# Kernel tuning notes

Hardware: AMD Instinct MI355X
Metric: run time of the kernel (lower is better)

The kernel has to match this reference:

```python
import jax, jax.numpy as jnp
import numpy as np

B, N, D, H, L, M = 2, 1024, 512, 8, 4, 256
DFF = 4 * D
LN_EPS = 1e-5


def layer_norm(x, g, b):
    mu = x.mean(-1, keepdims=True)
    var = x.var(-1, keepdims=True)
    return (x - mu) * jax.lax.rsqrt(var + LN_EPS) * g + b


def setup_inputs() -> dict:
    key = jax.random.key(0)
    ks = iter(jax.random.split(key, 32))
    s = 0.02
    inp = {
        "phi": jax.random.normal(next(ks), (B, N, D), jnp.float32),
        "coords": jax.random.normal(next(ks), (B, N, 3), jnp.float32),
        # CoordinateEncoding: Gaussian Fourier modes (init_std=0.05) + linear
        "modes": 0.05 * jax.random.normal(next(ks), (M, 3), jnp.float32),
        "We": s * jax.random.normal(next(ks), (2 * M, D), jnp.float32),
        "be": jnp.zeros((D,), jnp.float32),
        # per-block attention params, stacked over L blocks
        "wq": s * jax.random.normal(next(ks), (L, D, D), jnp.float32),
        "bq": jnp.zeros((L, D), jnp.float32),
        "wk": s * jax.random.normal(next(ks), (L, D, D), jnp.float32),
        "bk": jnp.zeros((L, D), jnp.float32),
        "wv": s * jax.random.normal(next(ks), (L, D, D), jnp.float32),
        "bv": jnp.zeros((L, D), jnp.float32),
        "wo": s * jax.random.normal(next(ks), (L, D, D), jnp.float32),
        "bo": jnp.zeros((L, D), jnp.float32),
        "temp": jnp.ones((L, H), jnp.float32),  # per-head distance temperature
        "ln1_g": jnp.ones((L, D), jnp.float32),
        "ln1_b": jnp.zeros((L, D), jnp.float32),
        "ln2_g": jnp.ones((L, D), jnp.float32),
        "ln2_b": jnp.zeros((L, D), jnp.float32),
        "w1": s * jax.random.normal(next(ks), (L, D, DFF), jnp.float32),
        "b1": jnp.zeros((L, DFF), jnp.float32),
        "w2": s * jax.random.normal(next(ks), (L, DFF, D), jnp.float32),
        "b2": jnp.zeros((L, D), jnp.float32),
        "fng": jnp.ones((D,), jnp.float32),
        "fnb": jnp.zeros((D,), jnp.float32),
    }
    return inp


def reference(phi, coords, modes, We, be, wq, bq, wk, bk, wv, bv, wo, bo, temp,
              ln1_g, ln1_b, ln2_g, ln2_b, w1, b1, w2, b2, fng, fnb):
    dh = D // H
    # coordinate encoding (random Fourier features)
    phase = jnp.einsum('bnc,mc->bnm', coords, modes)            # [B,N,M]
    feats = jnp.concatenate([jnp.cos(phase), jnp.sin(phase)], -1)  # [B,N,2M]
    x = phi + feats @ We + be
    # pairwise distances with epsilon shift, std-scaled per sample
    diff = coords[:, :, None, :] - (coords + 1e-5)[:, None, :, :]
    d = jnp.sqrt(jnp.sum(diff * diff, -1))                      # [B,N,N]
    d = d / jnp.std(d, axis=(-2, -1), keepdims=True, ddof=1)
    scale = 1.0 / np.sqrt(dh)
    for l in range(L):
        y = layer_norm(x, ln1_g[l], ln1_b[l])
        q = (y @ wq[l] + bq[l]).reshape(B, N, H, dh)
        k = (y @ wk[l] + bk[l]).reshape(B, N, H, dh)
        v = (y @ wv[l] + bv[l]).reshape(B, N, H, dh)
        scores = jnp.einsum('bihd,bjhd->bhij', q, k) * scale
        scores = scores - jax.nn.softplus(temp[l])[None, :, None, None] * d[:, None]
        a = jax.nn.softmax(scores, axis=-1)                     # [B,H,N,N]
        o = jnp.einsum('bhij,bjhd->bihd', a, v).reshape(B, N, D)
        x = x + o @ wo[l] + bo[l]
        z = layer_norm(x, ln2_g[l], ln2_b[l])
        h = jax.nn.gelu(z @ w1[l] + b1[l], approximate=False)
        x = x + h @ w2[l] + b2[l]
    return layer_norm(x, fng, fnb)
```

## Files before the change

kernel.cpp:

```cpp
#include <hip/hip_runtime.h>
#include <hip/hip_bf16.h>
#include <math.h>

#define BATCH 2
#define NTOK 1024
#define DMODEL 512
#define NHEAD 8
#define DH 64
#define NLAYER 4
#define MMODES 256
#define DFFN 2048

typedef unsigned short u16;
typedef __attribute__((ext_vector_type(4))) float f4;
typedef __attribute__((ext_vector_type(8))) short b8;

__device__ __forceinline__ float bf2f(u16 u) { return __uint_as_float(((unsigned)u) << 16); }
__device__ __forceinline__ u16 f2b(float x) {
    unsigned u = __float_as_uint(x);
    return (u16)((u + 0x7FFF + ((u >> 16) & 1)) >> 16);
}
__device__ __forceinline__ float ldx(const void* p, size_t i, int f32) {
    return f32 ? ((const float*)p)[i] : bf2f(((const u16*)p)[i]);
}
__device__ __forceinline__ void async_ld16(const u16* g, u16* l) {
    __builtin_amdgcn_global_load_lds((const __attribute__((address_space(1))) void*)g,
                                     (__attribute__((address_space(3))) void*)l, 16, 0, 0);
}

__global__ __launch_bounds__(256) void detect_kernel(const void* __restrict__ probe,
                                                     int* __restrict__ flag) {
    const u16* u = (const u16*)probe;
    int big = 0, zer = 0;
    for (int t = threadIdx.x; t < 768; t += 256) {
        u16 w = u[2 * t];
        int e = (w >> 7) & 0xFF;
        if (e >= 137) big++;
        if (w == 0) zer++;
    }
    __shared__ int sb, sz;
    if (threadIdx.x == 0) { sb = 0; sz = 0; }
    __syncthreads();
    atomicAdd(&sb, big);
    atomicAdd(&sz, zer);
    __syncthreads();
    if (threadIdx.x == 0) flag[0] = (sb >= 64 || sz >= 700) ? 1 : 0;
}

__global__ __launch_bounds__(256) void cvt_all_kernel(const void* __restrict__ phi,
                                                      const void* __restrict__ coords,
                                                      float* __restrict__ xf,
                                                      float* __restrict__ cf,
                                                      const int* __restrict__ fl) {
    int f = fl[0];
    int i = blockIdx.x * 256 + threadIdx.x;
    if (i < BATCH * NTOK * DMODEL) xf[i] = ldx(phi, i, f);
    if (i < BATCH * NTOK * 3) cf[i] = ldx(coords, i, f);
}

#define OB_BE 0
#define OB_BQKV 512
#define OB_BO 6656
#define OB_B1 8704
#define OB_B2 16896
#define OB_TEMP 18944
#define OB_L1G 18976
#define OB_L1B 21024
#define OB_L2G 23072
#define OB_L2B 25120
#define OB_FNG 27168
#define OB_FNB 27680
#define OB_MODES 28192
#define OB_TOTAL 28960
__global__ __launch_bounds__(256) void pack_params(
    const void* be_, const void* bq_, const void* bk_, const void* bv_,
    const void* bo_, const void* b1_, const void* b2_, const void* temp_,
    const void* l1g_, const void* l1b_, const void* l2g_, const void* l2b_,
    const void* fng_, const void* fnb_, const void* modes_,
    float* __restrict__ out, const int* __restrict__ fl) {
    int f = fl[0];
    for (int idx = blockIdx.x * 256 + threadIdx.x; idx < OB_TOTAL; idx += gridDim.x * 256) {
        float v;
        int i = idx;
        if (i < 512) v = ldx(be_, i, f);
        else if ((i -= 512) < 6144) {
            int l = i / 1536, r = i - l * 1536;
            v = (r < 512) ? ldx(bq_, (size_t)l * 512 + r, f)
              : (r < 1024) ? ldx(bk_, (size_t)l * 512 + r - 512, f)
              : ldx(bv_, (size_t)l * 512 + r - 1024, f);
        }
        else if ((i -= 6144) < 2048) v = ldx(bo_, i, f);
        else if ((i -= 2048) < 8192) v = ldx(b1_, i, f);
        else if ((i -= 8192) < 2048) v = ldx(b2_, i, f);
        else if ((i -= 2048) < 32)   v = ldx(temp_, i, f);
        else if ((i -= 32) < 2048)   v = ldx(l1g_, i, f);
        else if ((i -= 2048) < 2048) v = ldx(l1b_, i, f);
        else if ((i -= 2048) < 2048) v = ldx(l2g_, i, f);
        else if ((i -= 2048) < 2048) v = ldx(l2b_, i, f);
        else if ((i -= 2048) < 512)  v = ldx(fng_, i, f);
        else if ((i -= 512) < 512)   v = ldx(fnb_, i, f);
        else { i -= 512; v = ldx(modes_, i, f); }
        out[idx] = v;
    }
}

__device__ __forceinline__ void tr_tile(const void* src, size_t sbase, u16* dst,
                                        size_t dbase, int R, int C, int dstRowOff,
                                        int c0, int r0, int f) {
    __shared__ float t[32][33];
    int tx = threadIdx.x & 31, ty8 = threadIdx.x >> 5;
#pragma unroll
    for (int rr = 0; rr < 4; rr++) {
        int r = r0 + ty8 + rr * 8;
        t[ty8 + rr * 8][tx] = ldx(src, sbase + (size_t)r * C + c0 + tx, f);
    }
    __syncthreads();
#pragma unroll
    for (int rr = 0; rr < 4; rr++) {
        int c = c0 + ty8 + rr * 8;
        dst[dbase + (size_t)(dstRowOff + c) * R + r0 + tx] = f2b(t[tx][ty8 + rr * 8]);
    }
}
__global__ __launch_bounds__(256) void tr_all(const void* wq_, const void* wk_, const void* wv_,
                                              const void* wo_, const void* We_,
                                              const void* w1_, const void* w2_,
                                              u16* wqkvT, u16* woT, u16* WeT,
                                              u16* w1T, u16* w2T,
                                              const int* __restrict__ fl) {
    int f = fl[0];
    int z = blockIdx.x;
    if (z < 3072) {
        int mat = z >> 8, t = z & 255;
        int l = mat / 3, m3 = mat - l * 3;
        const void* s = (m3 == 0) ? wq_ : (m3 == 1) ? wk_ : wv_;
        tr_tile(s, (size_t)l * 512 * 512, wqkvT, (size_t)l * 1536 * 512,
                512, 512, m3 * 512, (t & 15) * 32, (t >> 4) * 32, f);
    } else if (z < 4096) {
        int zz = z - 3072, l = zz >> 8, t = zz & 255;
        tr_tile(wo_, (size_t)l * 512 * 512, woT, (size_t)l * 512 * 512,
                512, 512, 0, (t & 15) * 32, (t >> 4) * 32, f);
    } else if (z < 4352) {
        int t = z - 4096;
        tr_tile(We_, 0, WeT, 0, 512, 512, 0, (t & 15) * 32, (t >> 4) * 32, f);
    } else if (z < 8448) {
        int zz = z - 4352, l = zz >> 10, t = zz & 1023;
        tr_tile(w1_, (size_t)l * 512 * 2048, w1T, (size_t)l * 2048 * 512,
                512, 2048, 0, (t & 63) * 32, (t >> 6) * 32, f);
    } else {
        int zz = z - 8448, l = zz >> 10, t = zz & 1023;
        tr_tile(w2_, (size_t)l * 2048 * 512, w2T, (size_t)l * 512 * 2048,
                2048, 512, 0, (t & 15) * 32, (t >> 4) * 32, f);
    }
}

__global__ __launch_bounds__(256) void feats_dstat(const float* __restrict__ cf,
                                                   const float* __restrict__ modesF,
                                                   u16* __restrict__ ff,
                                                   float* __restrict__ part,
                                                   u16* __restrict__ dist) {
    int row = blockIdx.x;
    {
        int m = threadIdx.x;
        float cx = cf[row * 3 + 0], cy = cf[row * 3 + 1], cz = cf[row * 3 + 2];
        float ph = cx * modesF[m * 3 + 0] + cy * modesF[m * 3 + 1] + cz * modesF[m * 3 + 2];
        ff[(size_t)row * 512 + m] = f2b(cosf(ph));
        ff[(size_t)row * 512 + MMODES + m] = f2b(sinf(ph));
    }
    int b = row >> 10, i = row & 1023;
    const float* cb = cf + (size_t)b * NTOK * 3;
    float xi = cb[i * 3], yi = cb[i * 3 + 1], zi = cb[i * 3 + 2];
    float ls = 0.f, ls2 = 0.f;
    for (int j = threadIdx.x; j < NTOK; j += 256) {
        float dx = xi - (cb[j * 3] + 1e-5f);
        float dy = yi - (cb[j * 3 + 1] + 1e-5f);
        float dz = zi - (cb[j * 3 + 2] + 1e-5f);
        float d = sqrtf(dx * dx + dy * dy + dz * dz);
        if (dist) dist[(((size_t)row) << 10) + j] = f2b(d);
        ls += d; ls2 += d * d;
    }
    for (int off = 32; off; off >>= 1) {
        ls += __shfl_down(ls, off);
        ls2 += __shfl_down(ls2, off);
    }
    __shared__ float rs[4], rs2[4];
    int wid = threadIdx.x >> 6;
    if ((threadIdx.x & 63) == 0) { rs[wid] = ls; rs2[wid] = ls2; }
    __syncthreads();
    if (threadIdx.x == 0) {
        part[row] = rs[0] + rs[1] + rs[2] + rs[3];
        part[2048 + row] = rs2[0] + rs2[1] + rs2[2] + rs2[3];
    }
}
__global__ __launch_bounds__(256) void dreduce_kernel(const float* __restrict__ part,
                                                      float* __restrict__ inv_std) {
    int b = blockIdx.x;
    double s = 0.0, s2 = 0.0;
    for (int t = threadIdx.x; t < NTOK; t += 256) {
        s += (double)part[b * NTOK + t];
        s2 += (double)part[2048 + b * NTOK + t];
    }
    for (int off = 32; off; off >>= 1) {
        s += __shfl_down(s, off);
        s2 += __shfl_down(s2, off);
    }
    __shared__ double ds[4], ds2[4];
    int wid = threadIdx.x >> 6;
    if ((threadIdx.x & 63) == 0) { ds[wid] = s; ds2[wid] = s2; }
    __syncthreads();
    if (threadIdx.x == 0) {
        double S = ds[0] + ds[1] + ds[2] + ds[3];
        double S2 = ds2[0] + ds2[1] + ds2[2] + ds2[3];
        double n = (double)NTOK * (double)NTOK;
        double mean = S / n;
        double var = (S2 - n * mean * mean) / (n - 1.0);
        inv_std[b] = (float)(1.0 / sqrt(var));
    }
}

__global__ __launch_bounds__(256) void ln_bf_kernel(const float* __restrict__ x,
                                                    const float* __restrict__ gp,
                                                    const float* __restrict__ bp,
                                                    u16* __restrict__ y) {
    int row = blockIdx.x, tid = threadIdx.x;
    const float* xr = x + (size_t)row * DMODEL;
    float v0 = xr[tid], v1 = xr[tid + 256];
    float s = v0 + v1, s2 = v0 * v0 + v1 * v1;
    for (int off = 32; off; off >>= 1) {
        s += __shfl_down(s, off);
        s2 += __shfl_down(s2, off);
    }
    __shared__ float ls[4], ls2[4];
    int wid = tid >> 6;
    if ((tid & 63) == 0) { ls[wid] = s; ls2[wid] = s2; }
    __syncthreads();
    s = ls[0] + ls[1] + ls[2] + ls[3];
    s2 = ls2[0] + ls2[1] + ls2[2] + ls2[3];
    float mean = s * (1.0f / DMODEL);
    float var = s2 * (1.0f / DMODEL) - mean * mean;
    float r = rsqrtf(var + 1e-5f);
    y[(size_t)row * DMODEL + tid] = f2b((v0 - mean) * r * gp[tid] + bp[tid]);
    y[(size_t)row * DMODEL + tid + 256] = f2b((v1 - mean) * r * gp[tid + 256] + bp[tid + 256]);
}
__global__ __launch_bounds__(256) void ln_out_kernel(const float* __restrict__ x,
                                                     const float* __restrict__ gp,
                                                     const float* __restrict__ bp,
                                                     void* __restrict__ out,
                                                     const int* __restrict__ fl) {
    int f = fl[0];
    int row = blockIdx.x, tid = threadIdx.x;
    const float* xr = x + (size_t)row * DMODEL;
    float v0 = xr[tid], v1 = xr[tid + 256];
    float s = v0 + v1, s2 = v0 * v0 + v1 * v1;
    for (int off = 32; off; off >>= 1) {
        s += __shfl_down(s, off);
        s2 += __shfl_down(s2, off);
    }
    __shared__ float ls[4], ls2[4];
    int wid = tid >> 6;
    if ((tid & 63) == 0) { ls[wid] = s; ls2[wid] = s2; }
    __syncthreads();
    s = ls[0] + ls[1] + ls[2] + ls[3];
    s2 = ls2[0] + ls2[1] + ls2[2] + ls2[3];
    float mean = s * (1.0f / DMODEL);
    float var = s2 * (1.0f / DMODEL) - mean * mean;
    float r = rsqrtf(var + 1e-5f);
    float o0 = (v0 - mean) * r * gp[tid] + bp[tid];
    float o1 = (v1 - mean) * r * gp[tid + 256] + bp[tid + 256];
    size_t i0 = (size_t)row * DMODEL + tid;
    if (f) { ((float*)out)[i0] = o0; ((float*)out)[i0 + 256] = o1; }
    else   { ((u16*)out)[i0] = f2b(o0); ((u16*)out)[i0 + 256] = f2b(o1); }
}

template <int FM, int FN, int ACT, int RES, int OUTBF, int QKV>
__global__ __launch_bounds__(256) void gemm_mfma(const u16* __restrict__ A,
                                                 const u16* __restrict__ BT,
                                                 const float* __restrict__ bias,
                                                 const float* __restrict__ res,
                                                 void* __restrict__ Cp,
                                                 u16* __restrict__ VTp,
                                                 int M, int N, int K) {
    constexpr int BM = 32 * FM, BN = 32 * FN;
    constexpr int PA = BM / 64, PB = BN / 64;
    __shared__ u16 As[2 * BM * 32];
    __shared__ u16 Bs[2 * BN * 32];
    const int m0 = blockIdx.y * BM, n0 = blockIdx.x * BN;
    const int tid = threadIdx.x, lane = tid & 63, wid = tid >> 6;
    const int wm = (wid >> 1) * (16 * FM), wn = (wid & 1) * (16 * FN);
    const int quad = lane >> 4, low = lane & 15;
    const int srow = tid >> 2, scol = (tid & 3) * 8;
    f4 acc[FM][FN] = {};
    for (int k0 = 0; k0 < K; k0 += 64) {
#pragma unroll
        for (int ks = 0; ks < 2; ks++) {
#pragma unroll
            for (int p = 0; p < PA; p++)
                async_ld16(A + (size_t)(m0 + p * 64 + srow) * K + k0 + ks * 32 + scol,
                           As + ks * BM * 32 + p * 2048 + wid * 512);
#pragma unroll
            for (int p = 0; p < PB; p++)
                async_ld16(BT + (size_t)(n0 + p * 64 + srow) * K + k0 + ks * 32 + scol,
                           Bs + ks * BN * 32 + p * 2048 + wid * 512);
        }
        __syncthreads();
#pragma unroll
        for (int ks = 0; ks < 2; ks++) {
            b8 af[FM], bfr[FN];
#pragma unroll
            for (int i = 0; i < FM; i++)
                af[i] = *(const b8*)(As + ks * BM * 32 + (wm + i * 16 + low) * 32 + quad * 8);
#pragma unroll
            for (int j = 0; j < FN; j++)
                bfr[j] = *(const b8*)(Bs + ks * BN * 32 + (wn + j * 16 + low) * 32 + quad * 8);
#pragma unroll
            for (int i = 0; i < FM; i++)
#pragma unroll
                for (int j = 0; j < FN; j++)
                    acc[i][j] = __builtin_amdgcn_mfma_f32_16x16x32_bf16(af[i], bfr[j], acc[i][j], 0, 0, 0);
        }
        __syncthreads();
    }
#pragma unroll
    for (int i = 0; i < FM; i++) {
#pragma unroll
        for (int j = 0; j < FN; j++) {
            int gn = n0 + wn + j * 16 + low;
            float bv = bias[gn];
            if (QKV && gn >= 1024) {
                int h = (gn - 1024) >> 6, d = (gn - 1024) & 63;
                int gmb = m0 + wm + i * 16 + quad * 4;
                int bb = gmb >> 10, jj = gmb & 1023;
                ushort4 pk;
                pk.x = f2b(acc[i][j][0] + bv);
                pk.y = f2b(acc[i][j][1] + bv);
                pk.z = f2b(acc[i][j][2] + bv);
                pk.w = f2b(acc[i][j][3] + bv);
                *(ushort4*)(VTp + ((size_t)(bb * 8 + h) * 64 + d) * 1024 + jj) = pk;
            } else {
#pragma unroll
                for (int r = 0; r < 4; r++) {
                    int gm = m0 + wm + i * 16 + quad * 4 + r;
                    float v = acc[i][j][r] + bv;
                    if (ACT) v = 0.5f * v * (1.0f + erff(v * 0.70710678f));
                    if (RES) v += res[(size_t)gm * N + gn];
                    if (OUTBF) ((u16*)Cp)[(size_t)gm * N + gn] = f2b(v);
                    else       ((float*)Cp)[(size_t)gm * N + gn] = v;
                }
            }
        }
    }
}

template <int USE_DIST>
__global__ __launch_bounds__(256) void attn_mfma(const u16* __restrict__ qkv,
                                                 const u16* __restrict__ VT,
                                                 const float* __restrict__ cf,
                                                 const float* __restrict__ inv_std,
                                                 const float* __restrict__ tempF, int l,
                                                 const u16* __restrict__ dist,
                                                 u16* __restrict__ o) {
    const int it = blockIdx.x, h = blockIdx.y, b = blockIdx.z;
    const int i0 = it * 32, tid = threadIdx.x;
    const int lane = tid & 63, wid = tid >> 6;
    const int g = wid >> 1, p = wid & 1;
    const int quad = lane >> 4, low = lane & 15;
    __shared__ u16 Ks[2][64][72];
    __shared__ u16 Vs[2][64][72];
    __shared__ u16 Ps[4][16][72];
    __shared__ float s_ci[32][3];
    __shared__ float s_cj[2][64][3];
    const size_t rbase = (size_t)b * NTOK;
    const u16* VTh = VT + ((size_t)(b * 8 + h)) * 65536;
    b8 qf0, qf1;
    {
        const u16* qp = qkv + (rbase + i0 + g * 16 + low) * 1536 + h * 64;
        qf0 = *(const b8*)(qp + quad * 8);
        qf1 = *(const b8*)(qp + 32 + quad * 8);
    }
    if (!USE_DIST && tid < 32) {
        s_ci[tid][0] = cf[(rbase + i0 + tid) * 3 + 0];
        s_ci[tid][1] = cf[(rbase + i0 + tid) * 3 + 1];
        s_ci[tid][2] = cf[(rbase + i0 + tid) * 3 + 2];
    }
    float t0 = tempF[l * 8 + h];
    float spw = (fmaxf(t0, 0.f) + log1pf(__expf(-fabsf(t0)))) * inv_std[b];
    float mold[4] = {-1e30f, -1e30f, -1e30f, -1e30f};
    float lsum[4] = {0.f, 0.f, 0.f, 0.f};
    f4 oacc[4] = {};
    __syncthreads();
    float cqx[4], cqy[4], cqz[4];
    const u16* drow[4];
#pragma unroll
    for (int r = 0; r < 4; r++) {
        int ii = g * 16 + quad * 4 + r;
        if (USE_DIST) drow[r] = dist + ((rbase + i0 + ii) << 10);
        else { cqx[r] = s_ci[ii][0]; cqy[r] = s_ci[ii][1]; cqz[r] = s_ci[ii][2]; }
    }
    for (int t = 0; t < 8; t++) {
        __syncthreads();
#pragma unroll
        for (int tt = 0; tt < 2; tt++) {
            int j0s = (t * 2 + tt) * 64;
            int j = tid >> 2, dc = (tid & 3) * 16;
            const u16* kp = qkv + (rbase + j0s + j) * 1536 + 512 + h * 64 + dc;
            *(uint4*)&Ks[tt][j][dc] = *(const uint4*)kp;
            *(uint4*)&Ks[tt][j][dc + 8] = *(const uint4*)(kp + 8);
            const u16* vp = VTh + (size_t)j * 1024 + j0s + dc;
            *(uint4*)&Vs[tt][j][dc] = *(const uint4*)vp;
            *(uint4*)&Vs[tt][j][dc + 8] = *(const uint4*)(vp + 8);
            if (!USE_DIST && tid < 64) {
                s_cj[tt][tid][0] = cf[(rbase + j0s + tid) * 3 + 0] + 1e-5f;
                s_cj[tt][tid][1] = cf[(rbase + j0s + tid) * 3 + 1] + 1e-5f;
                s_cj[tt][tid][2] = cf[(rbase + j0s + tid) * 3 + 2] + 1e-5f;
            }
        }
        __syncthreads();
        const int j0 = (t * 2 + p) * 64;
        f4 sacc[4] = {};
#pragma unroll
        for (int jb = 0; jb < 4; jb++) {
            b8 bk0 = *(const b8*)&Ks[p][jb * 16 + low][quad * 8];
            b8 bk1 = *(const b8*)&Ks[p][jb * 16 + low][32 + quad * 8];
            sacc[jb] = __builtin_amdgcn_mfma_f32_16x16x32_bf16(qf0, bk0, sacc[jb], 0, 0, 0);
            sacc[jb] = __builtin_amdgcn_mfma_f32_16x16x32_bf16(qf1, bk1, sacc[jb], 0, 0, 0);
        }
        float sv[4][4];
#pragma unroll
        for (int jb = 0; jb < 4; jb++) {
            int j = jb * 16 + low;
            if (USE_DIST) {
#pragma unroll
                for (int r = 0; r < 4; r++)
                    sv[jb][r] = sacc[jb][r] * 0.125f - spw * bf2f(drow[r][j0 + j]);
            } else {
                float cjx = s_cj[p][j][0], cjy = s_cj[p][j][1], cjz = s_cj[p][j][2];
#pragma unroll
                for (int r = 0; r < 4; r++) {
                    float dx = cqx[r] - cjx, dy = cqy[r] - cjy, dz = cqz[r] - cjz;
                    sv[jb][r] = sacc[jb][r] * 0.125f - spw * sqrtf(dx * dx + dy * dy + dz * dz);
                }
            }
        }
        float alpha[4];
#pragma unroll
        for (int r = 0; r < 4; r++) {
            float mx = fmaxf(fmaxf(sv[0][r], sv[1][r]), fmaxf(sv[2][r], sv[3][r]));
            mx = fmaxf(mx, __shfl_xor(mx, 1));
            mx = fmaxf(mx, __shfl_xor(mx, 2));
            mx = fmaxf(mx, __shfl_xor(mx, 4));
            mx = fmaxf(mx, __shfl_xor(mx, 8));
            float mn = fmaxf(mold[r], mx);
            alpha[r] = __expf(mold[r] - mn);
            mold[r] = mn;
            float ps = 0.f;
#pragma unroll
            for (int jb = 0; jb < 4; jb++) {
                float pp = __expf(sv[jb][r] - mn);
                Ps[wid][quad * 4 + r][jb * 16 + low] = f2b(pp);
                ps += pp;
            }
            ps += __shfl_xor(ps, 1);
            ps += __shfl_xor(ps, 2);
            ps += __shfl_xor(ps, 4);
            ps += __shfl_xor(ps, 8);
            lsum[r] = lsum[r] * alpha[r] + ps;
        }
#pragma unroll
        for (int db = 0; db < 4; db++)
#pragma unroll
            for (int r = 0; r < 4; r++) oacc[db][r] *= alpha[r];
        b8 ap0 = *(const b8*)&Ps[wid][low][quad * 8];
        b8 ap1 = *(const b8*)&Ps[wid][low][32 + quad * 8];
#pragma unroll
        for (int db = 0; db < 4; db++) {
            b8 bv0 = *(const b8*)&Vs[p][db * 16 + low][quad * 8];
            b8 bv1 = *(const b8*)&Vs[p][db * 16 + low][32 + quad * 8];
            oacc[db] = __builtin_amdgcn_mfma_f32_16x16x32_bf16(ap0, bv0, oacc[db], 0, 0, 0);
            oacc[db] = __builtin_amdgcn_mfma_f32_16x16x32_bf16(ap1, bv1, oacc[db], 0, 0, 0);
        }
    }
    __syncthreads();
    float* scr = (float*)&Ks[0][0][0];
    float* Og = scr + g * 1088;
    float* Ml = Og + 1024;
    if (p == 1) {
#pragma unroll
        for (int db = 0; db < 4; db++)
#pragma unroll
            for (int r = 0; r < 4; r++)
                Og[(quad * 4 + r) * 64 + db * 16 + low] = oacc[db][r];
        if (low == 0) {
#pragma unroll
            for (int r = 0; r < 4; r++) {
                Ml[quad * 4 + r] = mold[r];
                Ml[16 + quad * 4 + r] = lsum[r];
            }
        }
    }
    __syncthreads();
    if (p == 0) {
#pragma unroll
        for (int r = 0; r < 4; r++) {
            int row = quad * 4 + r;
            float m1 = Ml[row], l1 = Ml[16 + row];
            float mm = fmaxf(mold[r], m1);
            float a0 = __expf(mold[r] - mm), a1 = __expf(m1 - mm);
            float rl = 1.f / (lsum[r] * a0 + l1 * a1);
            u16* op = o + (rbase + i0 + g * 16 + row) * 512 + h * 64 + low;
#pragma unroll
            for (int db = 0; db < 4; db++) {
                float v = oacc[db][r] * a0 + Og[row * 64 + db * 16 + low] * a1;
                op[db * 16] = f2b(v * rl);
            }
        }
    }
}

extern "C" void kernel_launch(void* const* d_in, const int* in_sizes, int n_in,
                              void* d_out, int out_size, void* d_ws, size_t ws_size,
                              hipStream_t stream) {
    const void* phi    = d_in[0];
    const void* coords = d_in[1];
    const void* modes  = d_in[2];
    const void* We     = d_in[3];
    const void* be     = d_in[4];
    const void* wq     = d_in[5];
    const void* bq     = d_in[6];
    const void* wk     = d_in[7];
    const void* bk     = d_in[8];
    const void* wv     = d_in[9];
    const void* bv     = d_in[10];
    const void* wo     = d_in[11];
    const void* bo     = d_in[12];
    const void* temp   = d_in[13];
    const void* ln1g   = d_in[14];
    const void* ln1b   = d_in[15];
    const void* ln2g   = d_in[16];
    const void* ln2b   = d_in[17];
    const void* w1     = d_in[18];
    const void* b1     = d_in[19];
    const void* w2     = d_in[20];
    const void* b2     = d_in[21];
    const void* fng    = d_in[22];
    const void* fnb    = d_in[23];

    const int R = BATCH * NTOK;
    char* ws = (char*)d_ws;
    const size_t MB = 1u << 20;
    float* xf   = (float*)(ws);
    u16*  yf    = (u16*)(ws + 4 * MB);
    u16*  of    = (u16*)(ws + 6 * MB);
    u16*  pool  = (u16*)(ws + 8 * MB);
    u16*  ff    = pool;
    u16*  qkvb  = pool;
    u16*  VTb   = (u16*)(ws + 14 * MB);
    u16*  hf    = pool;
    u16*  WeT   = (u16*)(ws + 16 * MB);
    u16*  wqkvT = (u16*)(ws + 16 * MB + 512 * 1024);
    u16*  woT   = (u16*)(ws + 22 * MB + 512 * 1024);
    u16*  w1T   = (u16*)(ws + 24 * MB + 512 * 1024);
    u16*  w2T   = (u16*)(ws + 32 * MB + 512 * 1024);
    float* prm  = (float*)(ws + 40 * MB + 512 * 1024);
    float* cf   = (float*)(ws + 41 * MB);
    float* part = (float*)(ws + 41 * MB + 128 * 1024);
    float* inv_std = (float*)(ws + 41 * MB + 192 * 1024);
    int*   flag = (int*)(ws + 41 * MB + 192 * 1024 + 64);
    u16* dist = (ws_size >= (size_t)46 * MB) ? (u16*)(ws + 42 * MB) : nullptr;

    detect_kernel<<<1, 256, 0, stream>>>(wq, flag);
    cvt_all_kernel<<<(R * DMODEL + 255) / 256, 256, 0, stream>>>(phi, coords, xf, cf, flag);
    pack_params<<<32, 256, 0, stream>>>(be, bq, bk, bv, bo, b1, b2, temp,
                                        ln1g, ln1b, ln2g, ln2b, fng, fnb, modes, prm, flag);
    tr_all<<<12544, 256, 0, stream>>>(wq, wk, wv, wo, We, w1, w2,
                                      wqkvT, woT, WeT, w1T, w2T, flag);

    feats_dstat<<<R, 256, 0, stream>>>(cf, prm + OB_MODES, ff, part, dist);
    dreduce_kernel<<<BATCH, 256, 0, stream>>>(part, inv_std);
    gemm_mfma<2, 2, 0, 1, 0, 0><<<dim3(8, 32), 256, 0, stream>>>(
        ff, WeT, prm + OB_BE, xf, xf, nullptr, R, DMODEL, DMODEL);

    for (int l = 0; l < NLAYER; l++) {
        ln_bf_kernel<<<R, 256, 0, stream>>>(xf, prm + OB_L1G + l * 512, prm + OB_L1B + l * 512, yf);
        gemm_mfma<2, 2, 0, 0, 1, 1><<<dim3(24, 32), 256, 0, stream>>>(
            yf, wqkvT + (size_t)l * 1536 * 512, prm + OB_BQKV + l * 1536, nullptr, qkvb, VTb,
            R, 1536, DMODEL);
        if (dist)
            attn_mfma<1><<<dim3(32, NHEAD, BATCH), 256, 0, stream>>>(
                qkvb, VTb, cf, inv_std, prm + OB_TEMP, l, dist, of);
        else
            attn_mfma<0><<<dim3(32, NHEAD, BATCH), 256, 0, stream>>>(
                qkvb, VTb, cf, inv_std, prm + OB_TEMP, l, nullptr, of);
        gemm_mfma<2, 2, 0, 1, 0, 0><<<dim3(8, 32), 256, 0, stream>>>(
            of, woT + (size_t)l * 512 * 512, prm + OB_BO + l * 512, xf, xf, nullptr,
            R, DMODEL, DMODEL);
        ln_bf_kernel<<<R, 256, 0, stream>>>(xf, prm + OB_L2G + l * 512, prm + OB_L2B + l * 512, yf);
        gemm_mfma<4, 2, 1, 0, 1, 0><<<dim3(32, 16), 256, 0, stream>>>(
            yf, w1T + (size_t)l * 2048 * 512, prm + OB_B1 + l * 2048, nullptr, hf, nullptr,
            R, DFFN, DMODEL);
        gemm_mfma<2, 2, 0, 1, 0, 0><<<dim3(8, 32), 256, 0, stream>>>(
            hf, w2T + (size_t)l * 512 * 2048, prm + OB_B2 + l * 512, xf, xf, nullptr,
            R, DMODEL, DFFN);
    }
    ln_out_kernel<<<R, 256, 0, stream>>>(xf, prm + OB_FNG, prm + OB_FNB, d_out, flag);
}
```

Baseline: 517.7 us.

## Fuse layer norms into GEMM prologues via epilogue row statistics; merge prep kernels

Residual-producing GEMMs now accumulate per-row sum and sum-of-squares with atomics in their epilogue. The following QKV and FFN1 GEMMs apply layer norm on the fly while loading the fp32 activations, which removes the standalone LN kernels and the bf16 intermediate buffer. The final LN also reuses these statistics. The detect, convert and param-pack kernels are merged into one prep kernel that also zeroes the stats buffer. The trade-offs are that the A tile is now a synchronous fp32 load instead of an async bf16 LDS load, there is atomic contention, and variance is computed as E[x²]−mean² in fp32.

New measurement: 582.9 us. +12.6%, slower.

```diff
diff --git a/kernel.cpp b/kernel.cpp
--- a/kernel.cpp
+++ b/kernel.cpp
@@ -28,8 +28,7 @@
                                      (__attribute__((address_space(3))) void*)l, 16, 0, 0);
 }
 
-__global__ __launch_bounds__(256) void detect_kernel(const void* __restrict__ probe,
-                                                     int* __restrict__ flag) {
+__device__ __forceinline__ int detect_local(const void* probe) {
     const u16* u = (const u16*)probe;
     int big = 0, zer = 0;
     for (int t = threadIdx.x; t < 768; t += 256) {
@@ -44,18 +43,7 @@
     atomicAdd(&sb, big);
     atomicAdd(&sz, zer);
     __syncthreads();
-    if (threadIdx.x == 0) flag[0] = (sb >= 64 || sz >= 700) ? 1 : 0;
-}
-
-__global__ __launch_bounds__(256) void cvt_all_kernel(const void* __restrict__ phi,
-                                                      const void* __restrict__ coords,
-                                                      float* __restrict__ xf,
-                                                      float* __restrict__ cf,
-                                                      const int* __restrict__ fl) {
-    int f = fl[0];
-    int i = blockIdx.x * 256 + threadIdx.x;
-    if (i < BATCH * NTOK * DMODEL) xf[i] = ldx(phi, i, f);
-    if (i < BATCH * NTOK * 3) cf[i] = ldx(coords, i, f);
+    return (sb >= 64 || sz >= 700) ? 1 : 0;
 }
 
 #define OB_BE 0
@@ -72,35 +60,51 @@
 #define OB_FNB 27680
 #define OB_MODES 28192
 #define OB_TOTAL 28960
-__global__ __launch_bounds__(256) void pack_params(
+
+__global__ __launch_bounds__(256) void prep_kernel(
+    const void* phi, const void* coords,
     const void* be_, const void* bq_, const void* bk_, const void* bv_,
     const void* bo_, const void* b1_, const void* b2_, const void* temp_,
     const void* l1g_, const void* l1b_, const void* l2g_, const void* l2b_,
     const void* fng_, const void* fnb_, const void* modes_,
-    float* __restrict__ out, const int* __restrict__ fl) {
-    int f = fl[0];
-    for (int idx = blockIdx.x * 256 + threadIdx.x; idx < OB_TOTAL; idx += gridDim.x * 256) {
-        float v;
-        int i = idx;
-        if (i < 512) v = ldx(be_, i, f);
-        else if ((i -= 512) < 6144) {
-            int l = i / 1536, r = i - l * 1536;
-            v = (r < 512) ? ldx(bq_, (size_t)l * 512 + r, f)
-              : (r < 1024) ? ldx(bk_, (size_t)l * 512 + r - 512, f)
-              : ldx(bv_, (size_t)l * 512 + r - 1024, f);
-        }
-        else if ((i -= 6144) < 2048) v = ldx(bo_, i, f);
-        else if ((i -= 2048) < 8192) v = ldx(b1_, i, f);
-        else if ((i -= 8192) < 2048) v = ldx(b2_, i, f);
-        else if ((i -= 2048) < 32)   v = ldx(temp_, i, f);
-        else if ((i -= 32) < 2048)   v = ldx(l1g_, i, f);
-        else if ((i -= 2048) < 2048) v = ldx(l1b_, i, f);
-        else if ((i -= 2048) < 2048) v = ldx(l2g_, i, f);
-        else if ((i -= 2048) < 2048) v = ldx(l2b_, i, f);
-        else if ((i -= 2048) < 512)  v = ldx(fng_, i, f);
-        else if ((i -= 512) < 512)   v = ldx(fnb_, i, f);
-        else { i -= 512; v = ldx(modes_, i, f); }
-        out[idx] = v;
+    const void* probe,
+    float* __restrict__ xf, float* __restrict__ cf, float* __restrict__ prm,
+    float* __restrict__ sbuf, int* __restrict__ flag) {
+    int f = detect_local(probe);
+    int z = blockIdx.x, tid = threadIdx.x;
+    if (z == 0 && tid == 0) flag[0] = f;
+    if (z < 4096) {
+        int i = z * 256 + tid;
+        if (i < BATCH * NTOK * DMODEL) xf[i] = ldx(phi, i, f);
+        if (i < BATCH * NTOK * 3) cf[i] = ldx(coords, i, f);
+    } else if (z < 4210) {
+        int idx = (z - 4096) * 256 + tid;
+        if (idx < OB_TOTAL) {
+            float v;
+            int i = idx;
+            if (i < 512) v = ldx(be_, i, f);
+            else if ((i -= 512) < 6144) {
+                int l = i / 1536, r = i - l * 1536;
+                v = (r < 512) ? ldx(bq_, (size_t)l * 512 + r, f)
+                  : (r < 1024) ? ldx(bk_, (size_t)l * 512 + r - 512, f)
+                  : ldx(bv_, (size_t)l * 512 + r - 1024, f);
+            }
+            else if ((i -= 6144) < 2048) v = ldx(bo_, i, f);
+            else if ((i -= 2048) < 8192) v = ldx(b1_, i, f);
+            else if ((i -= 8192) < 2048) v = ldx(b2_, i, f);
+            else if ((i -= 2048) < 32)   v = ldx(temp_, i, f);
+            else if ((i -= 32) < 2048)   v = ldx(l1g_, i, f);
+            else if ((i -= 2048) < 2048) v = ldx(l1b_, i, f);
+            else if ((i -= 2048) < 2048) v = ldx(l2g_, i, f);
+            else if ((i -= 2048) < 2048) v = ldx(l2b_, i, f);
+            else if ((i -= 2048) < 512)  v = ldx(fng_, i, f);
+            else if ((i -= 512) < 512)   v = ldx(fnb_, i, f);
+            else { i -= 512; v = ldx(modes_, i, f); }
+            prm[idx] = v;
+        }
+    } else {
+        int idx = (z - 4210) * 256 + tid;
+        sbuf[idx] = 0.f;
     }
 }
 
@@ -217,31 +221,8 @@
     }
 }
 
-__global__ __launch_bounds__(256) void ln_bf_kernel(const float* __restrict__ x,
-                                                    const float* __restrict__ gp,
-                                                    const float* __restrict__ bp,
-                                                    u16* __restrict__ y) {
-    int row = blockIdx.x, tid = threadIdx.x;
-    const float* xr = x + (size_t)row * DMODEL;
-    float v0 = xr[tid], v1 = xr[tid + 256];
-    float s = v0 + v1, s2 = v0 * v0 + v1 * v1;
-    for (int off = 32; off; off >>= 1) {
-        s += __shfl_down(s, off);
-        s2 += __shfl_down(s2, off);
-    }
-    __shared__ float ls[4], ls2[4];
-    int wid = tid >> 6;
-    if ((tid & 63) == 0) { ls[wid] = s; ls2[wid] = s2; }
-    __syncthreads();
-    s = ls[0] + ls[1] + ls[2] + ls[3];
-    s2 = ls2[0] + ls2[1] + ls2[2] + ls2[3];
-    float mean = s * (1.0f / DMODEL);
-    float var = s2 * (1.0f / DMODEL) - mean * mean;
-    float r = rsqrtf(var + 1e-5f);
-    y[(size_t)row * DMODEL + tid] = f2b((v0 - mean) * r * gp[tid] + bp[tid]);
-    y[(size_t)row * DMODEL + tid + 256] = f2b((v1 - mean) * r * gp[tid + 256] + bp[tid + 256]);
-}
 __global__ __launch_bounds__(256) void ln_out_kernel(const float* __restrict__ x,
+                                                     const float* __restrict__ sIn,
                                                      const float* __restrict__ gp,
                                                      const float* __restrict__ bp,
                                                      void* __restrict__ out,
@@ -249,21 +230,10 @@
     int f = fl[0];
     int row = blockIdx.x, tid = threadIdx.x;
     const float* xr = x + (size_t)row * DMODEL;
+    float mean = sIn[row * 2] * (1.0f / DMODEL);
+    float var = sIn[row * 2 + 1] * (1.0f / DMODEL) - mean * mean;
+    float r = rsqrtf(var + 1e-5f);
     float v0 = xr[tid], v1 = xr[tid + 256];
-    float s = v0 + v1, s2 = v0 * v0 + v1 * v1;
-    for (int off = 32; off; off >>= 1) {
-        s += __shfl_down(s, off);
-        s2 += __shfl_down(s2, off);
-    }
-    __shared__ float ls[4], ls2[4];
-    int wid = tid >> 6;
-    if ((tid & 63) == 0) { ls[wid] = s; ls2[wid] = s2; }
-    __syncthreads();
-    s = ls[0] + ls[1] + ls[2] + ls[3];
-    s2 = ls2[0] + ls2[1] + ls2[2] + ls2[3];
-    float mean = s * (1.0f / DMODEL);
-    float var = s2 * (1.0f / DMODEL) - mean * mean;
-    float r = rsqrtf(var + 1e-5f);
     float o0 = (v0 - mean) * r * gp[tid] + bp[tid];
     float o1 = (v1 - mean) * r * gp[tid + 256] + bp[tid + 256];
     size_t i0 = (size_t)row * DMODEL + tid;
@@ -271,13 +241,17 @@
     else   { ((u16*)out)[i0] = f2b(o0); ((u16*)out)[i0 + 256] = f2b(o1); }
 }
 
-template <int FM, int FN, int ACT, int RES, int OUTBF, int QKV>
-__global__ __launch_bounds__(256) void gemm_mfma(const u16* __restrict__ A,
+template <int FM, int FN, int ACT, int RES, int OUTBF, int QKV, int LNA, int STATS>
+__global__ __launch_bounds__(256) void gemm_mfma(const void* __restrict__ A,
                                                  const u16* __restrict__ BT,
                                                  const float* __restrict__ bias,
                                                  const float* __restrict__ res,
                                                  void* __restrict__ Cp,
                                                  u16* __restrict__ VTp,
+                                                 const float* __restrict__ sIn,
+                                                 const float* __restrict__ gIn,
+                                                 const float* __restrict__ bIn,
+                                                 float* __restrict__ sOut,
                                                  int M, int N, int K) {
     constexpr int BM = 32 * FM, BN = 32 * FN;
     constexpr int PA = BM / 64, PB = BN / 64;
@@ -288,17 +262,52 @@
     const int wm = (wid >> 1) * (16 * FM), wn = (wid & 1) * (16 * FN);
     const int quad = lane >> 4, low = lane & 15;
     const int srow = tid >> 2, scol = (tid & 3) * 8;
+    float meanp[PA], rstdp[PA];
+    const float* Af = (const float*)A;
+    if (LNA) {
+#pragma unroll
+        for (int p = 0; p < PA; p++) {
+            int row = m0 + p * 64 + srow;
+            float sm = sIn[row * 2] * (1.0f / DMODEL);
+            float sq = sIn[row * 2 + 1] * (1.0f / DMODEL);
+            meanp[p] = sm;
+            rstdp[p] = rsqrtf(sq - sm * sm + 1e-5f);
+        }
+    }
     f4 acc[FM][FN] = {};
     for (int k0 = 0; k0 < K; k0 += 64) {
 #pragma unroll
         for (int ks = 0; ks < 2; ks++) {
-#pragma unroll
-            for (int p = 0; p < PA; p++)
-                async_ld16(A + (size_t)(m0 + p * 64 + srow) * K + k0 + ks * 32 + scol,
-                           As + ks * BM * 32 + p * 2048 + wid * 512);
+            int kk = k0 + ks * 32 + scol;
+#pragma unroll
+            for (int p = 0; p < PA; p++) {
+                if (LNA) {
+                    const float* xr = Af + (size_t)(m0 + p * 64 + srow) * K + kk;
+                    float4 x0 = *(const float4*)xr;
+                    float4 x1 = *(const float4*)(xr + 4);
+                    float4 g0 = *(const float4*)(gIn + kk);
+                    float4 g1 = *(const float4*)(gIn + kk + 4);
+                    float4 b0 = *(const float4*)(bIn + kk);
+                    float4 b1 = *(const float4*)(bIn + kk + 4);
+                    float mn = meanp[p], rs = rstdp[p];
+                    u16 tmp[8];
+                    tmp[0] = f2b((x0.x - mn) * rs * g0.x + b0.x);
+                    tmp[1] = f2b((x0.y - mn) * rs * g0.y + b0.y);
+                    tmp[2] = f2b((x0.z - mn) * rs * g0.z + b0.z);
+                    tmp[3] = f2b((x0.w - mn) * rs * g0.w + b0.w);
+                    tmp[4] = f2b((x1.x - mn) * rs * g1.x + b1.x);
+                    tmp[5] = f2b((x1.y - mn) * rs * g1.y + b1.y);
+                    tmp[6] = f2b((x1.z - mn) * rs * g1.z + b1.z);
+                    tmp[7] = f2b((x1.w - mn) * rs * g1.w + b1.w);
+                    *(uint4*)(As + ks * BM * 32 + p * 2048 + tid * 8) = *(uint4*)tmp;
+                } else {
+                    async_ld16((const u16*)A + (size_t)(m0 + p * 64 + srow) * K + kk,
+                               As + ks * BM * 32 + p * 2048 + wid * 512);
+                }
+            }
 #pragma unroll
             for (int p = 0; p < PB; p++)
-                async_ld16(BT + (size_t)(n0 + p * 64 + srow) * K + k0 + ks * 32 + scol,
+                async_ld16(BT + (size_t)(n0 + p * 64 + srow) * K + kk,
                            Bs + ks * BN * 32 + p * 2048 + wid * 512);
         }
         __syncthreads();
@@ -318,6 +327,13 @@
                     acc[i][j] = __builtin_amdgcn_mfma_f32_16x16x32_bf16(af[i], bfr[j], acc[i][j], 0, 0, 0);
         }
         __syncthreads();
+    }
+    float rsum[FM][4], rsq[FM][4];
+    if (STATS) {
+#pragma unroll
+        for (int i = 0; i < FM; i++)
+#pragma unroll
+            for (int r = 0; r < 4; r++) { rsum[i][r] = 0.f; rsq[i][r] = 0.f; }
     }
 #pragma unroll
     for (int i = 0; i < FM; i++) {
@@ -344,9 +360,27 @@
                     if (RES) v += res[(size_t)gm * N + gn];
                     if (OUTBF) ((u16*)Cp)[(size_t)gm * N + gn] = f2b(v);
                     else       ((float*)Cp)[(size_t)gm * N + gn] = v;
+                    if (STATS) { rsum[i][r] += v; rsq[i][r] += v * v; }
                 }
             }
         }
+    }
+    if (STATS) {
+#pragma unroll
+        for (int i = 0; i < FM; i++)
+#pragma unroll
+            for (int r = 0; r < 4; r++) {
+                float a = rsum[i][r], q = rsq[i][r];
+                a += __shfl_xor(a, 1); q += __shfl_xor(q, 1);
+                a += __shfl_xor(a, 2); q += __shfl_xor(q, 2);
+                a += __shfl_xor(a, 4); q += __shfl_xor(q, 4);
+                a += __shfl_xor(a, 8); q += __shfl_xor(q, 8);
+                if (low == 0) {
+                    int row = m0 + wm + i * 16 + quad * 4 + r;
+                    atomicAdd(&sOut[row * 2], a);
+                    atomicAdd(&sOut[row * 2 + 1], q);
+                }
+            }
     }
 }
 
@@ -547,7 +581,6 @@
     char* ws = (char*)d_ws;
     const size_t MB = 1u << 20;
     float* xf   = (float*)(ws);
-    u16*  yf    = (u16*)(ws + 4 * MB);
     u16*  of    = (u16*)(ws + 6 * MB);
     u16*  pool  = (u16*)(ws + 8 * MB);
     u16*  ff    = pool;
@@ -564,24 +597,27 @@
     float* part = (float*)(ws + 41 * MB + 128 * 1024);
     float* inv_std = (float*)(ws + 41 * MB + 192 * 1024);
     int*   flag = (int*)(ws + 41 * MB + 192 * 1024 + 64);
+    float* sbuf = (float*)(ws + 41 * MB + 256 * 1024);
     u16* dist = (ws_size >= (size_t)46 * MB) ? (u16*)(ws + 42 * MB) : nullptr;
 
-    detect_kernel<<<1, 256, 0, stream>>>(wq, flag);
-    cvt_all_kernel<<<(R * DMODEL + 255) / 256, 256, 0, stream>>>(phi, coords, xf, cf, flag);
-    pack_params<<<32, 256, 0, stream>>>(be, bq, bk, bv, bo, b1, b2, temp,
-                                        ln1g, ln1b, ln2g, ln2b, fng, fnb, modes, prm, flag);
+    prep_kernel<<<4354, 256, 0, stream>>>(phi, coords, be, bq, bk, bv, bo, b1, b2, temp,
+                                          ln1g, ln1b, ln2g, ln2b, fng, fnb, modes, wq,
+                                          xf, cf, prm, sbuf, flag);
     tr_all<<<12544, 256, 0, stream>>>(wq, wk, wv, wo, We, w1, w2,
                                       wqkvT, woT, WeT, w1T, w2T, flag);
-
     feats_dstat<<<R, 256, 0, stream>>>(cf, prm + OB_MODES, ff, part, dist);
     dreduce_kernel<<<BATCH, 256, 0, stream>>>(part, inv_std);
-    gemm_mfma<2, 2, 0, 1, 0, 0><<<dim3(8, 32), 256, 0, stream>>>(
-        ff, WeT, prm + OB_BE, xf, xf, nullptr, R, DMODEL, DMODEL);
+    gemm_mfma<2, 2, 0, 1, 0, 0, 0, 1><<<dim3(8, 32), 256, 0, stream>>>(
+        ff, WeT, prm + OB_BE, xf, xf, nullptr, nullptr, nullptr, nullptr, sbuf,
+        R, DMODEL, DMODEL);
 
     for (int l = 0; l < NLAYER; l++) {
-        ln_bf_kernel<<<R, 256, 0, stream>>>(xf, prm + OB_L1G + l * 512, prm + OB_L1B + l * 512, yf);
-        gemm_mfma<2, 2, 0, 0, 1, 1><<<dim3(24, 32), 256, 0, stream>>>(
-            yf, wqkvT + (size_t)l * 1536 * 512, prm + OB_BQKV + l * 1536, nullptr, qkvb, VTb,
+        float* Sin1 = sbuf + (size_t)(2 * l) * 4096;
+        float* Sow  = sbuf + (size_t)(2 * l + 1) * 4096;
+        float* Sow2 = sbuf + (size_t)(2 * l + 2) * 4096;
+        gemm_mfma<2, 2, 0, 0, 1, 1, 1, 0><<<dim3(24, 32), 256, 0, stream>>>(
+            xf, wqkvT + (size_t)l * 1536 * 512, prm + OB_BQKV + l * 1536, nullptr, qkvb, VTb,
+            Sin1, prm + OB_L1G + l * 512, prm + OB_L1B + l * 512, nullptr,
             R, 1536, DMODEL);
         if (dist)
             attn_mfma<1><<<dim3(32, NHEAD, BATCH), 256, 0, stream>>>(
@@ -589,16 +625,17 @@
         else
             attn_mfma<0><<<dim3(32, NHEAD, BATCH), 256, 0, stream>>>(
                 qkvb, VTb, cf, inv_std, prm + OB_TEMP, l, nullptr, of);
-        gemm_mfma<2, 2, 0, 1, 0, 0><<<dim3(8, 32), 256, 0, stream>>>(
+        gemm_mfma<2, 2, 0, 1, 0, 0, 0, 1><<<dim3(8, 32), 256, 0, stream>>>(
             of, woT + (size_t)l * 512 * 512, prm + OB_BO + l * 512, xf, xf, nullptr,
-            R, DMODEL, DMODEL);
-        ln_bf_kernel<<<R, 256, 0, stream>>>(xf, prm + OB_L2G + l * 512, prm + OB_L2B + l * 512, yf);
-        gemm_mfma<4, 2, 1, 0, 1, 0><<<dim3(32, 16), 256, 0, stream>>>(
-            yf, w1T + (size_t)l * 2048 * 512, prm + OB_B1 + l * 2048, nullptr, hf, nullptr,
+            nullptr, nullptr, nullptr, Sow, R, DMODEL, DMODEL);
+        gemm_mfma<4, 2, 1, 0, 1, 0, 1, 0><<<dim3(32, 16), 256, 0, stream>>>(
+            xf, w1T + (size_t)l * 2048 * 512, prm + OB_B1 + l * 2048, nullptr, hf, nullptr,
+            Sow, prm + OB_L2G + l * 512, prm + OB_L2B + l * 512, nullptr,
             R, DFFN, DMODEL);
-        gemm_mfma<2, 2, 0, 1, 0, 0><<<dim3(8, 32), 256, 0, stream>>>(
+        gemm_mfma<2, 2, 0, 1, 0, 0, 0, 1><<<dim3(8, 32), 256, 0, stream>>>(
             hf, w2T + (size_t)l * 512 * 2048, prm + OB_B2 + l * 512, xf, xf, nullptr,
-            R, DMODEL, DFFN);
-    }
-    ln_out_kernel<<<R, 256, 0, stream>>>(xf, prm + OB_FNG, prm + OB_FNB, d_out, flag);
-}
+            nullptr, nullptr, nullptr, Sow2, R, DMODEL, DFFN);
+    }
+    ln_out_kernel<<<R, 256, 0, stream>>>(xf, sbuf + (size_t)(2 * NLAYER) * 4096,
+                                         prm + OB_FNG, prm + OB_FNB, d_out, flag);
+}
```

## Split-K with atomic accumulation for residual GEMMs; merge prep kernels

Applied to the files above, without the earlier changes.

The Wo and W2 projections, which add into the fp32 residual stream, now run as split-K GEMMs (2 and 4 slices). Each slice atomically adds its partial sum into xf, and only slice zero adds the bias. This raises the block count from 256 so more compute units are busy, at the cost of atomic traffic and a nondeterministic summation order. Separately, the detect, convert and param-pack kernels are merged into one launch that recomputes the dtype flag in every block.

New measurement: 536.2 us. +3.6%, slower.

```diff
diff --git a/kernel.cpp b/kernel.cpp
--- a/kernel.cpp
+++ b/kernel.cpp
@@ -28,8 +28,7 @@
                                      (__attribute__((address_space(3))) void*)l, 16, 0, 0);
 }
 
-__global__ __launch_bounds__(256) void detect_kernel(const void* __restrict__ probe,
-                                                     int* __restrict__ flag) {
+__device__ __forceinline__ int detect_local(const void* probe) {
     const u16* u = (const u16*)probe;
     int big = 0, zer = 0;
     for (int t = threadIdx.x; t < 768; t += 256) {
@@ -44,18 +43,7 @@
     atomicAdd(&sb, big);
     atomicAdd(&sz, zer);
     __syncthreads();
-    if (threadIdx.x == 0) flag[0] = (sb >= 64 || sz >= 700) ? 1 : 0;
-}
-
-__global__ __launch_bounds__(256) void cvt_all_kernel(const void* __restrict__ phi,
-                                                      const void* __restrict__ coords,
-                                                      float* __restrict__ xf,
-                                                      float* __restrict__ cf,
-                                                      const int* __restrict__ fl) {
-    int f = fl[0];
-    int i = blockIdx.x * 256 + threadIdx.x;
-    if (i < BATCH * NTOK * DMODEL) xf[i] = ldx(phi, i, f);
-    if (i < BATCH * NTOK * 3) cf[i] = ldx(coords, i, f);
+    return (sb >= 64 || sz >= 700) ? 1 : 0;
 }
 
 #define OB_BE 0
@@ -72,35 +60,48 @@
 #define OB_FNB 27680
 #define OB_MODES 28192
 #define OB_TOTAL 28960
-__global__ __launch_bounds__(256) void pack_params(
+
+__global__ __launch_bounds__(256) void prep_kernel(
+    const void* phi, const void* coords,
     const void* be_, const void* bq_, const void* bk_, const void* bv_,
     const void* bo_, const void* b1_, const void* b2_, const void* temp_,
     const void* l1g_, const void* l1b_, const void* l2g_, const void* l2b_,
     const void* fng_, const void* fnb_, const void* modes_,
-    float* __restrict__ out, const int* __restrict__ fl) {
-    int f = fl[0];
-    for (int idx = blockIdx.x * 256 + threadIdx.x; idx < OB_TOTAL; idx += gridDim.x * 256) {
-        float v;
-        int i = idx;
-        if (i < 512) v = ldx(be_, i, f);
-        else if ((i -= 512) < 6144) {
-            int l = i / 1536, r = i - l * 1536;
-            v = (r < 512) ? ldx(bq_, (size_t)l * 512 + r, f)
-              : (r < 1024) ? ldx(bk_, (size_t)l * 512 + r - 512, f)
-              : ldx(bv_, (size_t)l * 512 + r - 1024, f);
-        }
-        else if ((i -= 6144) < 2048) v = ldx(bo_, i, f);
-        else if ((i -= 2048) < 8192) v = ldx(b1_, i, f);
-        else if ((i -= 8192) < 2048) v = ldx(b2_, i, f);
-        else if ((i -= 2048) < 32)   v = ldx(temp_, i, f);
-        else if ((i -= 32) < 2048)   v = ldx(l1g_, i, f);
-        else if ((i -= 2048) < 2048) v = ldx(l1b_, i, f);
-        else if ((i -= 2048) < 2048) v = ldx(l2g_, i, f);
-        else if ((i -= 2048) < 2048) v = ldx(l2b_, i, f);
-        else if ((i -= 2048) < 512)  v = ldx(fng_, i, f);
-        else if ((i -= 512) < 512)   v = ldx(fnb_, i, f);
-        else { i -= 512; v = ldx(modes_, i, f); }
-        out[idx] = v;
+    const void* probe,
+    float* __restrict__ xf, float* __restrict__ cf, float* __restrict__ prm,
+    int* __restrict__ flag) {
+    int f = detect_local(probe);
+    int z = blockIdx.x, tid = threadIdx.x;
+    if (z == 0 && tid == 0) flag[0] = f;
+    if (z < 4096) {
+        int i = z * 256 + tid;
+        if (i < BATCH * NTOK * DMODEL) xf[i] = ldx(phi, i, f);
+        if (i < BATCH * NTOK * 3) cf[i] = ldx(coords, i, f);
+    } else {
+        int idx = (z - 4096) * 256 + tid;
+        if (idx < OB_TOTAL) {
+            float v;
+            int i = idx;
+            if (i < 512) v = ldx(be_, i, f);
+            else if ((i -= 512) < 6144) {
+                int l = i / 1536, r = i - l * 1536;
+                v = (r < 512) ? ldx(bq_, (size_t)l * 512 + r, f)
+                  : (r < 1024) ? ldx(bk_, (size_t)l * 512 + r - 512, f)
+                  : ldx(bv_, (size_t)l * 512 + r - 1024, f);
+            }
+            else if ((i -= 6144) < 2048) v = ldx(bo_, i, f);
+            else if ((i -= 2048) < 8192) v = ldx(b1_, i, f);
+            else if ((i -= 8192) < 2048) v = ldx(b2_, i, f);
+            else if ((i -= 2048) < 32)   v = ldx(temp_, i, f);
+            else if ((i -= 32) < 2048)   v = ldx(l1g_, i, f);
+            else if ((i -= 2048) < 2048) v = ldx(l1b_, i, f);
+            else if ((i -= 2048) < 2048) v = ldx(l2g_, i, f);
+            else if ((i -= 2048) < 2048) v = ldx(l2b_, i, f);
+            else if ((i -= 2048) < 512)  v = ldx(fng_, i, f);
+            else if ((i -= 512) < 512)   v = ldx(fnb_, i, f);
+            else { i -= 512; v = ldx(modes_, i, f); }
+            prm[idx] = v;
+        }
     }
 }
 
@@ -271,7 +272,7 @@
     else   { ((u16*)out)[i0] = f2b(o0); ((u16*)out)[i0 + 256] = f2b(o1); }
 }
 
-template <int FM, int FN, int ACT, int RES, int OUTBF, int QKV>
+template <int FM, int FN, int ACT, int RES, int OUTBF, int QKV, int ATOM, int SPLITK>
 __global__ __launch_bounds__(256) void gemm_mfma(const u16* __restrict__ A,
                                                  const u16* __restrict__ BT,
                                                  const float* __restrict__ bias,
@@ -284,21 +285,24 @@
     __shared__ u16 As[2 * BM * 32];
     __shared__ u16 Bs[2 * BN * 32];
     const int m0 = blockIdx.y * BM, n0 = blockIdx.x * BN;
+    const int kslice = (SPLITK > 1) ? (K / SPLITK) : K;
+    const int kbeg = (SPLITK > 1) ? blockIdx.z * kslice : 0;
     const int tid = threadIdx.x, lane = tid & 63, wid = tid >> 6;
     const int wm = (wid >> 1) * (16 * FM), wn = (wid & 1) * (16 * FN);
     const int quad = lane >> 4, low = lane & 15;
     const int srow = tid >> 2, scol = (tid & 3) * 8;
     f4 acc[FM][FN] = {};
-    for (int k0 = 0; k0 < K; k0 += 64) {
+    for (int k0 = kbeg; k0 < kbeg + kslice; k0 += 64) {
 #pragma unroll
         for (int ks = 0; ks < 2; ks++) {
+            int kk = k0 + ks * 32 + scol;
 #pragma unroll
             for (int p = 0; p < PA; p++)
-                async_ld16(A + (size_t)(m0 + p * 64 + srow) * K + k0 + ks * 32 + scol,
+                async_ld16(A + (size_t)(m0 + p * 64 + srow) * K + kk,
                            As + ks * BM * 32 + p * 2048 + wid * 512);
 #pragma unroll
             for (int p = 0; p < PB; p++)
-                async_ld16(BT + (size_t)(n0 + p * 64 + srow) * K + k0 + ks * 32 + scol,
+                async_ld16(BT + (size_t)(n0 + p * 64 + srow) * K + kk,
                            Bs + ks * BN * 32 + p * 2048 + wid * 512);
         }
         __syncthreads();
@@ -335,6 +339,14 @@
                 pk.z = f2b(acc[i][j][2] + bv);
                 pk.w = f2b(acc[i][j][3] + bv);
                 *(ushort4*)(VTp + ((size_t)(bb * 8 + h) * 64 + d) * 1024 + jj) = pk;
+            } else if (ATOM) {
+#pragma unroll
+                for (int r = 0; r < 4; r++) {
+                    int gm = m0 + wm + i * 16 + quad * 4 + r;
+                    float v = acc[i][j][r];
+                    if (blockIdx.z == 0) v += bv;
+                    atomicAdd(&((float*)Cp)[(size_t)gm * N + gn], v);
+                }
             } else {
 #pragma unroll
                 for (int r = 0; r < 4; r++) {
@@ -566,21 +578,19 @@
     int*   flag = (int*)(ws + 41 * MB + 192 * 1024 + 64);
     u16* dist = (ws_size >= (size_t)46 * MB) ? (u16*)(ws + 42 * MB) : nullptr;
 
-    detect_kernel<<<1, 256, 0, stream>>>(wq, flag);
-    cvt_all_kernel<<<(R * DMODEL + 255) / 256, 256, 0, stream>>>(phi, coords, xf, cf, flag);
-    pack_params<<<32, 256, 0, stream>>>(be, bq, bk, bv, bo, b1, b2, temp,
-                                        ln1g, ln1b, ln2g, ln2b, fng, fnb, modes, prm, flag);
+    prep_kernel<<<4210, 256, 0, stream>>>(phi, coords, be, bq, bk, bv, bo, b1, b2, temp,
+                                          ln1g, ln1b, ln2g, ln2b, fng, fnb, modes, wq,
+                                          xf, cf, prm, flag);
     tr_all<<<12544, 256, 0, stream>>>(wq, wk, wv, wo, We, w1, w2,
                                       wqkvT, woT, WeT, w1T, w2T, flag);
-
     feats_dstat<<<R, 256, 0, stream>>>(cf, prm + OB_MODES, ff, part, dist);
     dreduce_kernel<<<BATCH, 256, 0, stream>>>(part, inv_std);
-    gemm_mfma<2, 2, 0, 1, 0, 0><<<dim3(8, 32), 256, 0, stream>>>(
+    gemm_mfma<2, 2, 0, 1, 0, 0, 0, 0><<<dim3(8, 32), 256, 0, stream>>>(
         ff, WeT, prm + OB_BE, xf, xf, nullptr, R, DMODEL, DMODEL);
 
     for (int l = 0; l < NLAYER; l++) {
         ln_bf_kernel<<<R, 256, 0, stream>>>(xf, prm + OB_L1G + l * 512, prm + OB_L1B + l * 512, yf);
-        gemm_mfma<2, 2, 0, 0, 1, 1><<<dim3(24, 32), 256, 0, stream>>>(
+        gemm_mfma<2, 2, 0, 0, 1, 1, 0, 0><<<dim3(24, 32), 256, 0, stream>>>(
             yf, wqkvT + (size_t)l * 1536 * 512, prm + OB_BQKV + l * 1536, nullptr, qkvb, VTb,
             R, 1536, DMODEL);
         if (dist)
@@ -589,15 +599,15 @@
         else
             attn_mfma<0><<<dim3(32, NHEAD, BATCH), 256, 0, stream>>>(
                 qkvb, VTb, cf, inv_std, prm + OB_TEMP, l, nullptr, of);
-        gemm_mfma<2, 2, 0, 1, 0, 0><<<dim3(8, 32), 256, 0, stream>>>(
-            of, woT + (size_t)l * 512 * 512, prm + OB_BO + l * 512, xf, xf, nullptr,
+        gemm_mfma<2, 2, 0, 0, 0, 0, 1, 2><<<dim3(8, 32, 2), 256, 0, stream>>>(
+            of, woT + (size_t)l * 512 * 512, prm + OB_BO + l * 512, nullptr, xf, nullptr,
             R, DMODEL, DMODEL);
         ln_bf_kernel<<<R, 256, 0, stream>>>(xf, prm + OB_L2G + l * 512, prm + OB_L2B + l * 512, yf);
-        gemm_mfma<4, 2, 1, 0, 1, 0><<<dim3(32, 16), 256, 0, stream>>>(
+        gemm_mfma<4, 2, 1, 0, 1, 0, 0, 0><<<dim3(32, 16), 256, 0, stream>>>(
             yf, w1T + (size_t)l * 2048 * 512, prm + OB_B1 + l * 2048, nullptr, hf, nullptr,
             R, DFFN, DMODEL);
-        gemm_mfma<2, 2, 0, 1, 0, 0><<<dim3(8, 32), 256, 0, stream>>>(
-            hf, w2T + (size_t)l * 512 * 2048, prm + OB_B2 + l * 512, xf, xf, nullptr,
+        gemm_mfma<2, 2, 0, 0, 0, 0, 1, 4><<<dim3(8, 32, 4), 256, 0, stream>>>(
+            hf, w2T + (size_t)l * 512 * 2048, prm + OB_B2 + l * 512, nullptr, xf, nullptr,
             R, DMODEL, DFFN);
     }
     ln_out_kernel<<<R, 256, 0, stream>>>(xf, prm + OB_FNG, prm + OB_FNB, d_out, flag);
```
